# Kernel tuning notes

Hardware: AMD Instinct MI355X
Metric: run time of the kernel (lower is better)

The kernel has to match this reference:

```python
import jax, jax.numpy as jnp
import numpy as np

B, N, D, C = 4, 8192, 256, 1000
EPS = 1e-5


def expmap0(x, c=-1.0, eps=EPS):
    # Poincare-ball exponential map at the origin (matches torch version).
    x_norm = jnp.maximum(jnp.linalg.norm(x, axis=-1, keepdims=True), eps)
    curve_norm = jnp.sqrt(-c) * x_norm
    scale = jnp.tanh(curve_norm) / curve_norm
    return scale * x


def setup_inputs() -> dict:
    key = jax.random.key(0)
    k1, k2, k3 = jax.random.split(key, 3)
    features = jax.random.normal(k1, (B, N, D), dtype=jnp.float32)
    # kaiming-uniform-like scale for a 256-fan-in linear / embedding table
    lim = 1.0 / np.sqrt(D)
    W = jax.random.uniform(k2, (D, D), dtype=jnp.float32, minval=-lim, maxval=lim)
    b = jnp.zeros((D,), dtype=jnp.float32)
    embeddings = jax.random.uniform(k3, (C, D), dtype=jnp.float32, minval=-lim, maxval=lim)
    logit_scale = jnp.zeros((), dtype=jnp.float32)  # log(1.0)
    return {"features": features, "W": W, "b": b,
            "embeddings": embeddings, "logit_scale": logit_scale}


def reference(features, W, b, embeddings, logit_scale):
    # projection (nn.Linear): y = x @ W^T + b
    x = jnp.einsum("bnd,ed->bne", features, W) + b
    # map features and prototypes onto the Poincare ball (curvature = -1)
    x = expmap0(x)                       # [B, N, D], norms < 1
    protos = expmap0(embeddings)         # [C, D],    norms < 1

    # pairwise Poincare distance, computed via the norm expansion
    x_sq = jnp.sum(x * x, axis=-1)               # [B, N]
    p_sq = jnp.sum(protos * protos, axis=-1)     # [C]
    xp = jnp.einsum("bnd,cd->bnc", x, protos)    # [B, N, C]
    diff_sq = jnp.maximum(x_sq[..., None] + p_sq[None, None, :] - 2.0 * xp, 0.0)

    denom = jnp.maximum((1.0 - x_sq)[..., None] * (1.0 - p_sq)[None, None, :], EPS)
    argument = jnp.maximum(1.0 + 2.0 * diff_sq / denom, 1.0 + EPS)
    dists = jnp.arccosh(argument)                # [B, N, C]

    scale = jnp.minimum(jnp.exp(logit_scale), 100.0)
    return -dists * scale
```

## Files before the change

kernel.cpp:

```cpp
#include <hip/hip_runtime.h>
#include <hip/hip_fp16.h>


#define EPSF 1e-5f

typedef _Float16 half8 __attribute__((ext_vector_type(8)));
typedef _Float16 half4v __attribute__((ext_vector_type(4)));
typedef float f32x4 __attribute__((ext_vector_type(4)));

typedef __attribute__((address_space(3))) unsigned int as3_u32;
typedef __attribute__((address_space(1))) unsigned int as1_u32;
#define GLOAD16(gp, lp) __builtin_amdgcn_global_load_lds(  \
    (const as1_u32*)(gp), (as3_u32*)(lp), 16, 0, 0)

static __device__ __forceinline__ f32x4 mfma16(half8 a, half8 b, f32x4 c) {
  return __builtin_amdgcn_mfma_f32_16x16x32_f16(a, b, c, 0, 0, 0);
}

#define PROTO_OFF 0
#define PSQ_OFF   (1024 * 512)
#define WS_BYTES  (PSQ_OFF + 4096)

__global__ __launch_bounds__(256) void prep_kernel(const float* __restrict__ emb,
                                                   char* __restrict__ ws) {
  const int tid = threadIdx.x;
  const int wave = tid >> 6, lane = tid & 63;
  const int row = blockIdx.x * 4 + wave;
  float4 v = {0.f, 0.f, 0.f, 0.f};
  if (row < 1000) v = ((const float4*)emb)[row * 64 + lane];
  float s = v.x * v.x + v.y * v.y + v.z * v.z + v.w * v.w;
#pragma unroll
  for (int m = 1; m < 64; m <<= 1) s += __shfl_xor(s, m, 64);
  float r  = sqrtf(s);
  float rc = fmaxf(r, EPSF);
  float e  = __expf(2.0f * rc);
  float t  = 1.0f - 2.0f / (e + 1.0f);
  float sc = t / rc;
  float ps = t * t;
  if (row >= 1000) { sc = 0.0f; ps = 0.0f; }
  half4v h;
  h[0] = (_Float16)(v.x * sc); h[1] = (_Float16)(v.y * sc);
  h[2] = (_Float16)(v.z * sc); h[3] = (_Float16)(v.w * sc);
  const int byte = (lane * 8) ^ ((row & 7) << 4);
  *(half4v*)(ws + PROTO_OFF + row * 512 + byte) = h;
  if (lane == 0) ((float*)(ws + PSQ_OFF))[row] = ps;
}

__global__ __launch_bounds__(256, 2) void fused_kernel(
    const float* __restrict__ fea, const float* __restrict__ W,
    const float* __restrict__ bvec, const float* __restrict__ lsc,
    const char* __restrict__ ws, float* __restrict__ out) {
  __shared__ char lds[65536];
  char* buf0 = lds;
  char* buf1 = lds + 32768;

  const int tid  = threadIdx.x;
  const int w    = tid >> 6, lane = tid & 63;
  const int g = lane >> 4, i = lane & 15;
  const int xr = (i & 7) << 4;
  const int m0 = blockIdx.x * 64;

  const char*  pimg  = ws + PROTO_OFF;
  const float* psq_g = (const float*)(ws + PSQ_OFF);

  const f32x4 z4 = {0.f, 0.f, 0.f, 0.f};
  f32x4 accW[16];
#pragma unroll
  for (int cf = 0; cf < 16; ++cf) accW[cf] = z4;

  auto stageW = [&](int c, char* dst) {
#pragma unroll
    for (int p = 0; p < 8; ++p) {
      const int u = p * 256 + tid;
      const int n = u >> 3, k8 = u & 7;
      const float4* src = (const float4*)(W + (size_t)n * 256 + c * 64 + k8 * 8);
      float4 v0 = src[0], v1 = src[1];
      half8 h = {(_Float16)v0.x, (_Float16)v0.y, (_Float16)v0.z, (_Float16)v0.w,
                 (_Float16)v1.x, (_Float16)v1.y, (_Float16)v1.z, (_Float16)v1.w};
      *(half8*)(dst + n * 128 + ((k8 * 16) ^ ((n & 7) << 4))) = h;
    }
  };
  auto mfmaW = [&](int c, const char* bsrc) {
#pragma unroll
    for (int ksl = 0; ksl < 2; ++ksl) {
      const float4* ap = (const float4*)(fea +
          (size_t)(m0 + w * 16 + i) * 256 + c * 64 + ksl * 32 + g * 8);
      float4 a0 = ap[0], a1 = ap[1];
      half8 a = {(_Float16)a0.x, (_Float16)a0.y, (_Float16)a0.z, (_Float16)a0.w,
                 (_Float16)a1.x, (_Float16)a1.y, (_Float16)a1.z, (_Float16)a1.w};
#pragma unroll
      for (int cf = 0; cf < 16; ++cf) {
        half8 b = *(const half8*)(bsrc + (cf * 16 + i) * 128 +
                                  ((ksl * 64 + g * 16) ^ xr));
        accW[cf] = mfma16(a, b, accW[cf]);
      }
    }
  };

  stageW(0, buf0); __syncthreads();
  stageW(1, buf1); mfmaW(0, buf0); __syncthreads();
  stageW(2, buf0); mfmaW(1, buf1); __syncthreads();
  stageW(3, buf1); mfmaW(2, buf0); __syncthreads();
  mfmaW(3, buf1);  __syncthreads();

  auto stageP = [&](int nt, char* dst) {
#pragma unroll
    for (int p = 0; p < 8; ++p) {
      const int chunk = p * 4 + w;
      GLOAD16(pimg + (size_t)nt * 32768 + chunk * 1024 + lane * 16,
              dst + chunk * 1024);
    }
  };
  stageP(0, buf1);

  float ssum[4] = {0.f, 0.f, 0.f, 0.f};
#pragma unroll
  for (int cf = 0; cf < 16; ++cf) {
    const float bc = bvec[cf * 16 + i];
#pragma unroll
    for (int r = 0; r < 4; ++r) {
      accW[cf][r] += bc;
      ssum[r] = fmaf(accW[cf][r], accW[cf][r], ssum[r]);
    }
  }
#pragma unroll
  for (int m = 1; m < 16; m <<= 1)
#pragma unroll
    for (int r = 0; r < 4; ++r) ssum[r] += __shfl_xor(ssum[r], m, 64);

  float scl[4], xsv[4];
#pragma unroll
  for (int r = 0; r < 4; ++r) {
    float rn = sqrtf(ssum[r]);
    float rc = fmaxf(rn, EPSF);
    float e  = __expf(2.0f * rc);
    float t  = 1.0f - 2.0f / (e + 1.0f);
    scl[r] = t / rc;
    xsv[r] = t * t;
  }

  char* xsl = buf0 + w * 8192;
#pragma unroll
  for (int cf = 0; cf < 16; ++cf)
#pragma unroll
    for (int r = 0; r < 4; ++r) {
      const int row = g * 4 + r;
      *(_Float16*)(xsl + row * 512 + (((cf * 16 + i) * 2) ^ ((row & 7) << 4))) =
          (_Float16)(accW[cf][r] * scl[r]);
    }
  half8 A[8];
#pragma unroll
  for (int ks = 0; ks < 8; ++ks)
    A[ks] = *(const half8*)(xsl + i * 512 + ((ks * 64 + g * 16) ^ xr));

  const float sc_ln2 = fminf(__expf(lsc[0]), 100.0f) * 0.69314718055994531f;

  asm volatile("s_waitcnt vmcnt(0) lgkmcnt(0)" ::: "memory");
  __builtin_amdgcn_s_barrier();
  __builtin_amdgcn_sched_barrier(0);

  auto stepP = [&](int nt, const char* cur, char* nxt) {
    float psq[4];
#pragma unroll
    for (int cf = 0; cf < 4; ++cf) psq[cf] = psq_g[nt * 64 + cf * 16 + i];

    if (nt < 15) stageP(nt + 1, nxt);

    f32x4 acc[4] = {z4, z4, z4, z4};
#pragma unroll
    for (int ks = 0; ks < 8; ++ks) {
#pragma unroll
      for (int cf = 0; cf < 4; ++cf) {
        half8 b = *(const half8*)(cur + (cf * 16 + i) * 512 +
                                  ((ks * 64 + g * 16) ^ xr));
        acc[cf] = mfma16(A[ks], b, acc[cf]);
      }
    }
#pragma unroll
    for (int cf = 0; cf < 4; ++cf) {
      const float ps = psq[cf], omp = 1.0f - ps;
      const int col = nt * 64 + cf * 16 + i;
#pragma unroll
      for (int r = 0; r < 4; ++r) {
        const float xs   = xsv[r];
        const float diff = fmaxf(fmaf(-2.0f, acc[cf][r], xs + ps), 0.0f);
        const float den  = fmaxf((1.0f - xs) * omp, EPSF);
        const float arg  = fmaxf(fmaf(2.0f * diff, __builtin_amdgcn_rcpf(den), 1.0f),
                                 1.0f + EPSF);
        const float sq   = __builtin_amdgcn_sqrtf(fmaf(arg, arg, -1.0f));
        const float dist = __log2f(arg + sq);
        if (col < 1000)
          out[(size_t)(m0 + w * 16 + g * 4 + r) * 1000 + col] = -dist * sc_ln2;
      }
    }
    if (nt < 15) {
      asm volatile("s_waitcnt vmcnt(16)" ::: "memory");
      __builtin_amdgcn_s_barrier();
      __builtin_amdgcn_sched_barrier(0);
    }
  };

  for (int nt2 = 0; nt2 < 16; nt2 += 2) {
    stepP(nt2,     buf1, buf0);
    stepP(nt2 + 1, buf0, buf1);
  }
}

__global__ __launch_bounds__(256) void fallback_kernel(
    const float* __restrict__ fea, const float* __restrict__ W,
    const float* __restrict__ b, const float* __restrict__ emb,
    const float* __restrict__ lsc, float* __restrict__ out) {
  __shared__ float fr_[16][256];
  __shared__ float xr_[16][256];
  __shared__ float xs_[16];
  const int tid  = threadIdx.x;
  const int row0 = blockIdx.x * 16;

  for (int u = tid; u < 16 * 256; u += 256)
    fr_[u >> 8][u & 255] = fea[(size_t)(row0 + (u >> 8)) * 256 + (u & 255)];
  __syncthreads();

  float acc[16];
  const float bj = b[tid];
#pragma unroll
  for (int r = 0; r < 16; ++r) acc[r] = bj;
  for (int k = 0; k < 256; ++k) {
    const float wv = W[(size_t)tid * 256 + k];
#pragma unroll
    for (int r = 0; r < 16; ++r) acc[r] = fmaf(fr_[r][k], wv, acc[r]);
  }
#pragma unroll
  for (int r = 0; r < 16; ++r) xr_[r][tid] = acc[r];
  __syncthreads();

  if (tid < 16) {
    float s = 0.f;
    for (int k = 0; k < 256; ++k) s = fmaf(xr_[tid][k], xr_[tid][k], s);
    const float rn = sqrtf(s), rc = fmaxf(rn, EPSF);
    const float e = __expf(2.f * rc), t = 1.f - 2.f / (e + 1.f);
    xs_[tid] = t * t;
    fr_[tid][0] = t / rc;
  }
  __syncthreads();
  for (int u = tid; u < 16 * 256; u += 256)
    xr_[u >> 8][u & 255] *= fr_[u >> 8][0];
  __syncthreads();

  const float sc_out = fminf(__expf(lsc[0]), 100.0f);
  for (int c = tid; c < 1000; c += 256) {
    float s = 0.f;
    for (int k = 0; k < 256; ++k) {
      const float e0 = emb[(size_t)c * 256 + k];
      s = fmaf(e0, e0, s);
    }
    const float rn = sqrtf(s), rc = fmaxf(rn, EPSF);
    const float e = __expf(2.f * rc), t = 1.f - 2.f / (e + 1.f);
    const float psc = t / rc, ps = t * t, omp = 1.f - ps;
    float dots[16];
#pragma unroll
    for (int r = 0; r < 16; ++r) dots[r] = 0.f;
    for (int k = 0; k < 256; ++k) {
      const float pk = emb[(size_t)c * 256 + k] * psc;
#pragma unroll
      for (int r = 0; r < 16; ++r) dots[r] = fmaf(xr_[r][k], pk, dots[r]);
    }
#pragma unroll
    for (int r = 0; r < 16; ++r) {
      const float xs = xs_[r];
      const float diff = fmaxf(xs + ps - 2.f * dots[r], 0.f);
      const float den  = fmaxf((1.f - xs) * omp, EPSF);
      const float arg  = fmaxf(1.f + 2.f * diff / den, 1.f + EPSF);
      const float d    = logf(arg + sqrtf(fmaf(arg, arg, -1.f)));
      out[(size_t)(row0 + r) * 1000 + c] = -d * sc_out;
    }
  }
}

extern "C" void kernel_launch(void* const* d_in, const int* in_sizes, int n_in,
                              void* d_out, int out_size, void* d_ws, size_t ws_size,
                              hipStream_t stream) {
  (void)in_sizes; (void)n_in; (void)out_size;
  const float* fea = (const float*)d_in[0];
  const float* W   = (const float*)d_in[1];
  const float* b   = (const float*)d_in[2];
  const float* emb = (const float*)d_in[3];
  const float* ls  = (const float*)d_in[4];
  float* out = (float*)d_out;
  char*  ws  = (char*)d_ws;

  if (ws_size >= (size_t)WS_BYTES) {
    prep_kernel<<<256, 256, 0, stream>>>(emb, ws);
    fused_kernel<<<512, 256, 0, stream>>>(fea, W, b, ls, ws, out);
  } else {
    fallback_kernel<<<2048, 256, 0, stream>>>(fea, W, b, emb, ls, out);
  }
}
```

Measured before the change: 190.2 us.

## Split fused kernel across 8 waves with column halves and LDS-shared norms

Doubles the block to 512 threads, giving each pair of waves one 16-row strip, with each wave handling half of the projection output columns and half of the prototype columns. Partial squared norms are exchanged through LDS to finish the expmap scale. Prototype squared norms are staged in LDS once instead of being read from global memory every tile. The goal is more waves per CU to hide latency in the distance phase. The cost is more barriers and 70 KB of dynamic LDS per block, which caps blocks per CU and may contradict the 4-block launch bound.

```diff
diff --git a/kernel.cpp b/kernel.cpp
--- a/kernel.cpp
+++ b/kernel.cpp
@@ -8,11 +8,18 @@
 typedef _Float16 half4v __attribute__((ext_vector_type(4)));
 typedef float f32x4 __attribute__((ext_vector_type(4)));
 
+typedef __attribute__((address_space(3))) char as3_char;
 typedef __attribute__((address_space(3))) unsigned int as3_u32;
 typedef __attribute__((address_space(1))) unsigned int as1_u32;
 #define GLOAD16(gp, lp) __builtin_amdgcn_global_load_lds(  \
     (const as1_u32*)(gp), (as3_u32*)(lp), 16, 0, 0)
 
+#define LDS_H8(off)  (*((__attribute__((address_space(3)))       half8*)((as3_char*)lds + (off))))
+#define LDS_CH8(off) (*((__attribute__((address_space(3))) const half8*)((as3_char*)lds + (off))))
+#define LDS_F16(off) (*((__attribute__((address_space(3)))    _Float16*)((as3_char*)lds + (off))))
+#define LDS_F32(off) (*((__attribute__((address_space(3)))       float*)((as3_char*)lds + (off))))
+#define LDS_V4(off)  (*((__attribute__((address_space(3)))       f32x4*)((as3_char*)lds + (off))))
+
 static __device__ __forceinline__ f32x4 mfma16(half8 a, half8 b, f32x4 c) {
   return __builtin_amdgcn_mfma_f32_16x16x32_f16(a, b, c, 0, 0, 0);
 }
@@ -20,6 +27,10 @@
 #define PROTO_OFF 0
 #define PSQ_OFF   (1024 * 512)
 #define WS_BYTES  (PSQ_OFF + 4096)
+
+#define PSQ_L   65536
+#define PSUM_L  69632
+#define LDS_SZ  70144
 
 __global__ __launch_bounds__(256) void prep_kernel(const float* __restrict__ emb,
                                                    char* __restrict__ ws) {
@@ -46,163 +57,176 @@
   if (lane == 0) ((float*)(ws + PSQ_OFF))[row] = ps;
 }
 
-__global__ __launch_bounds__(256, 2) void fused_kernel(
+__global__ __launch_bounds__(512, 4) void fused_kernel(
     const float* __restrict__ fea, const float* __restrict__ W,
     const float* __restrict__ bvec, const float* __restrict__ lsc,
     const char* __restrict__ ws, float* __restrict__ out) {
-  __shared__ char lds[65536];
-  char* buf0 = lds;
-  char* buf1 = lds + 32768;
-
+  extern __shared__ char lds[];
   const int tid  = threadIdx.x;
-  const int w    = tid >> 6, lane = tid & 63;
+  const int wave = tid >> 6, lane = tid & 63;
+  const int r = wave >> 1, c = wave & 1;
   const int g = lane >> 4, i = lane & 15;
   const int xr = (i & 7) << 4;
+  const int ht = r * 64 + lane;
   const int m0 = blockIdx.x * 64;
-
-  const char*  pimg  = ws + PROTO_OFF;
-  const float* psq_g = (const float*)(ws + PSQ_OFF);
+  const int cbase = c * 32768;
+
+  const char* pimg = ws + PROTO_OFF;
+
+  float bl[8];
+#pragma unroll
+  for (int cf = 0; cf < 8; ++cf) bl[cf] = bvec[c * 128 + cf * 16 + i];
+  const float sc_ln2 = fminf(__expf(lsc[0]), 100.0f) * 0.69314718055994531f;
+  if (tid < 256) {
+    f32x4 pq = ((const f32x4*)(ws + PSQ_OFF))[tid];
+    LDS_V4(PSQ_L + tid * 16) = pq;
+  }
 
   const f32x4 z4 = {0.f, 0.f, 0.f, 0.f};
-  f32x4 accW[16];
-#pragma unroll
-  for (int cf = 0; cf < 16; ++cf) accW[cf] = z4;
-
-  auto stageW = [&](int c, char* dst) {
-#pragma unroll
-    for (int p = 0; p < 8; ++p) {
-      const int u = p * 256 + tid;
-      const int n = u >> 3, k8 = u & 7;
-      const float4* src = (const float4*)(W + (size_t)n * 256 + c * 64 + k8 * 8);
+  f32x4 accW[8];
+#pragma unroll
+  for (int cf = 0; cf < 8; ++cf) accW[cf] = z4;
+
+  auto stageW = [&](int kc, int boff) {
+#pragma unroll
+    for (int p = 0; p < 4; ++p) {
+      const int u = p * 256 + ht;
+      const int nl = u >> 3, k8 = u & 7;
+      const float4* src = (const float4*)(W + (size_t)(c * 128 + nl) * 256 +
+                                          kc * 64 + k8 * 8);
       float4 v0 = src[0], v1 = src[1];
       half8 h = {(_Float16)v0.x, (_Float16)v0.y, (_Float16)v0.z, (_Float16)v0.w,
                  (_Float16)v1.x, (_Float16)v1.y, (_Float16)v1.z, (_Float16)v1.w};
-      *(half8*)(dst + n * 128 + ((k8 * 16) ^ ((n & 7) << 4))) = h;
+      LDS_H8(boff + nl * 128 + ((k8 * 16) ^ ((nl & 7) << 4))) = h;
     }
   };
-  auto mfmaW = [&](int c, const char* bsrc) {
+  auto mfmaW = [&](int kc, int boff) {
 #pragma unroll
     for (int ksl = 0; ksl < 2; ++ksl) {
-      const float4* ap = (const float4*)(fea +
-          (size_t)(m0 + w * 16 + i) * 256 + c * 64 + ksl * 32 + g * 8);
+      const float4* ap = (const float4*)(fea + (size_t)(m0 + r * 16 + i) * 256 +
+                                         kc * 64 + ksl * 32 + g * 8);
       float4 a0 = ap[0], a1 = ap[1];
       half8 a = {(_Float16)a0.x, (_Float16)a0.y, (_Float16)a0.z, (_Float16)a0.w,
                  (_Float16)a1.x, (_Float16)a1.y, (_Float16)a1.z, (_Float16)a1.w};
 #pragma unroll
-      for (int cf = 0; cf < 16; ++cf) {
-        half8 b = *(const half8*)(bsrc + (cf * 16 + i) * 128 +
-                                  ((ksl * 64 + g * 16) ^ xr));
+      for (int cf = 0; cf < 8; ++cf) {
+        half8 b = LDS_CH8(boff + (cf * 16 + i) * 128 + ((ksl * 64 + g * 16) ^ xr));
         accW[cf] = mfma16(a, b, accW[cf]);
       }
     }
   };
 
-  stageW(0, buf0); __syncthreads();
-  stageW(1, buf1); mfmaW(0, buf0); __syncthreads();
-  stageW(2, buf0); mfmaW(1, buf1); __syncthreads();
-  stageW(3, buf1); mfmaW(2, buf0); __syncthreads();
-  mfmaW(3, buf1);  __syncthreads();
-
-  auto stageP = [&](int nt, char* dst) {
-#pragma unroll
-    for (int p = 0; p < 8; ++p) {
-      const int chunk = p * 4 + w;
-      GLOAD16(pimg + (size_t)nt * 32768 + chunk * 1024 + lane * 16,
-              dst + chunk * 1024);
-    }
-  };
-  stageP(0, buf1);
+  stageW(0, cbase);         __syncthreads();
+  stageW(1, cbase + 16384); mfmaW(0, cbase);         __syncthreads();
+  stageW(2, cbase);         mfmaW(1, cbase + 16384); __syncthreads();
+  stageW(3, cbase + 16384); mfmaW(2, cbase);         __syncthreads();
+  mfmaW(3, cbase + 16384);  __syncthreads();
 
   float ssum[4] = {0.f, 0.f, 0.f, 0.f};
 #pragma unroll
-  for (int cf = 0; cf < 16; ++cf) {
-    const float bc = bvec[cf * 16 + i];
-#pragma unroll
-    for (int r = 0; r < 4; ++r) {
-      accW[cf][r] += bc;
-      ssum[r] = fmaf(accW[cf][r], accW[cf][r], ssum[r]);
-    }
-  }
+  for (int cf = 0; cf < 8; ++cf)
+#pragma unroll
+    for (int reg = 0; reg < 4; ++reg) {
+      accW[cf][reg] += bl[cf];
+      ssum[reg] = fmaf(accW[cf][reg], accW[cf][reg], ssum[reg]);
+    }
 #pragma unroll
   for (int m = 1; m < 16; m <<= 1)
 #pragma unroll
-    for (int r = 0; r < 4; ++r) ssum[r] += __shfl_xor(ssum[r], m, 64);
+    for (int reg = 0; reg < 4; ++reg) ssum[reg] += __shfl_xor(ssum[reg], m, 64);
+  if (i == 0) {
+#pragma unroll
+    for (int reg = 0; reg < 4; ++reg)
+      LDS_F32(PSUM_L + (c * 64 + r * 16 + g * 4 + reg) * 4) = ssum[reg];
+  }
+  __syncthreads();
 
   float scl[4], xsv[4];
 #pragma unroll
-  for (int r = 0; r < 4; ++r) {
-    float rn = sqrtf(ssum[r]);
+  for (int reg = 0; reg < 4; ++reg) {
+    const int row = r * 16 + g * 4 + reg;
+    float s  = LDS_F32(PSUM_L + row * 4) + LDS_F32(PSUM_L + (64 + row) * 4);
+    float rn = sqrtf(s);
     float rc = fmaxf(rn, EPSF);
     float e  = __expf(2.0f * rc);
     float t  = 1.0f - 2.0f / (e + 1.0f);
-    scl[r] = t / rc;
-    xsv[r] = t * t;
-  }
-
-  char* xsl = buf0 + w * 8192;
-#pragma unroll
-  for (int cf = 0; cf < 16; ++cf)
-#pragma unroll
-    for (int r = 0; r < 4; ++r) {
-      const int row = g * 4 + r;
-      *(_Float16*)(xsl + row * 512 + (((cf * 16 + i) * 2) ^ ((row & 7) << 4))) =
-          (_Float16)(accW[cf][r] * scl[r]);
-    }
+    scl[reg] = t / rc;
+    xsv[reg] = t * t;
+  }
+
+#pragma unroll
+  for (int cf = 0; cf < 8; ++cf)
+#pragma unroll
+    for (int reg = 0; reg < 4; ++reg) {
+      const int row = r * 16 + g * 4 + reg;
+      const int col = c * 128 + cf * 16 + i;
+      LDS_F16(row * 512 + ((col * 2) ^ ((row & 7) << 4))) =
+          (_Float16)(accW[cf][reg] * scl[reg]);
+    }
+  __syncthreads();
   half8 A[8];
 #pragma unroll
   for (int ks = 0; ks < 8; ++ks)
-    A[ks] = *(const half8*)(xsl + i * 512 + ((ks * 64 + g * 16) ^ xr));
-
-  const float sc_ln2 = fminf(__expf(lsc[0]), 100.0f) * 0.69314718055994531f;
-
-  asm volatile("s_waitcnt vmcnt(0) lgkmcnt(0)" ::: "memory");
+    A[ks] = LDS_CH8((r * 16 + i) * 512 + ((ks * 64 + g * 16) ^ xr));
+  asm volatile("s_waitcnt lgkmcnt(0)" ::: "memory");
+  __builtin_amdgcn_sched_barrier(0);
+  __syncthreads();
+
+  auto stageP = [&](int t, int boff) {
+#pragma unroll
+    for (int p = 0; p < 4; ++p) {
+      const int chunk = p * 4 + r;
+      GLOAD16(pimg + ((size_t)(c * 512 + t * 32) * 512) + chunk * 1024 + lane * 16,
+              (as3_char*)lds + boff + chunk * 1024);
+    }
+  };
+  stageP(0, cbase);
+  asm volatile("s_waitcnt vmcnt(0)" ::: "memory");
   __builtin_amdgcn_s_barrier();
   __builtin_amdgcn_sched_barrier(0);
 
-  auto stepP = [&](int nt, const char* cur, char* nxt) {
-    float psq[4];
-#pragma unroll
-    for (int cf = 0; cf < 4; ++cf) psq[cf] = psq_g[nt * 64 + cf * 16 + i];
-
-    if (nt < 15) stageP(nt + 1, nxt);
-
-    f32x4 acc[4] = {z4, z4, z4, z4};
-#pragma unroll
-    for (int ks = 0; ks < 8; ++ks) {
-#pragma unroll
-      for (int cf = 0; cf < 4; ++cf) {
-        half8 b = *(const half8*)(cur + (cf * 16 + i) * 512 +
-                                  ((ks * 64 + g * 16) ^ xr));
+  for (int t = 0; t < 16; ++t) {
+    const int cur = cbase + (t & 1) * 16384;
+    const int nxt = cbase + ((t + 1) & 1) * 16384;
+
+    float psq[2];
+#pragma unroll
+    for (int cf = 0; cf < 2; ++cf)
+      psq[cf] = LDS_F32(PSQ_L + (c * 512 + t * 32 + cf * 16 + i) * 4);
+
+    if (t < 15) stageP(t + 1, nxt);
+
+    f32x4 acc[2] = {z4, z4};
+#pragma unroll
+    for (int ks = 0; ks < 8; ++ks)
+#pragma unroll
+      for (int cf = 0; cf < 2; ++cf) {
+        half8 b = LDS_CH8(cur + (cf * 16 + i) * 512 + ((ks * 64 + g * 16) ^ xr));
         acc[cf] = mfma16(A[ks], b, acc[cf]);
       }
-    }
-#pragma unroll
-    for (int cf = 0; cf < 4; ++cf) {
+
+#pragma unroll
+    for (int cf = 0; cf < 2; ++cf) {
       const float ps = psq[cf], omp = 1.0f - ps;
-      const int col = nt * 64 + cf * 16 + i;
-#pragma unroll
-      for (int r = 0; r < 4; ++r) {
-        const float xs   = xsv[r];
-        const float diff = fmaxf(fmaf(-2.0f, acc[cf][r], xs + ps), 0.0f);
+      const int col = c * 512 + t * 32 + cf * 16 + i;
+#pragma unroll
+      for (int reg = 0; reg < 4; ++reg) {
+        const float xs   = xsv[reg];
+        const float diff = fmaxf(fmaf(-2.0f, acc[cf][reg], xs + ps), 0.0f);
         const float den  = fmaxf((1.0f - xs) * omp, EPSF);
         const float arg  = fmaxf(fmaf(2.0f * diff, __builtin_amdgcn_rcpf(den), 1.0f),
                                  1.0f + EPSF);
         const float sq   = __builtin_amdgcn_sqrtf(fmaf(arg, arg, -1.0f));
         const float dist = __log2f(arg + sq);
         if (col < 1000)
-          out[(size_t)(m0 + w * 16 + g * 4 + r) * 1000 + col] = -dist * sc_ln2;
+          out[(size_t)(m0 + r * 16 + g * 4 + reg) * 1000 + col] = -dist * sc_ln2;
       }
     }
-    if (nt < 15) {
-      asm volatile("s_waitcnt vmcnt(16)" ::: "memory");
+    if (t < 15) {
+      asm volatile("s_waitcnt vmcnt(8)" ::: "memory");
       __builtin_amdgcn_s_barrier();
       __builtin_amdgcn_sched_barrier(0);
     }
-  };
-
-  for (int nt2 = 0; nt2 < 16; nt2 += 2) {
-    stepP(nt2,     buf1, buf0);
-    stepP(nt2 + 1, buf0, buf1);
   }
 }
 
@@ -247,10 +271,10 @@
   __syncthreads();
 
   const float sc_out = fminf(__expf(lsc[0]), 100.0f);
-  for (int c = tid; c < 1000; c += 256) {
+  for (int cc = tid; cc < 1000; cc += 256) {
     float s = 0.f;
     for (int k = 0; k < 256; ++k) {
-      const float e0 = emb[(size_t)c * 256 + k];
+      const float e0 = emb[(size_t)cc * 256 + k];
       s = fmaf(e0, e0, s);
     }
     const float rn = sqrtf(s), rc = fmaxf(rn, EPSF);
@@ -260,7 +284,7 @@
 #pragma unroll
     for (int r = 0; r < 16; ++r) dots[r] = 0.f;
     for (int k = 0; k < 256; ++k) {
-      const float pk = emb[(size_t)c * 256 + k] * psc;
+      const float pk = emb[(size_t)cc * 256 + k] * psc;
 #pragma unroll
       for (int r = 0; r < 16; ++r) dots[r] = fmaf(xr_[r][k], pk, dots[r]);
     }
@@ -271,7 +295,7 @@
       const float den  = fmaxf((1.f - xs) * omp, EPSF);
       const float arg  = fmaxf(1.f + 2.f * diff / den, 1.f + EPSF);
       const float d    = logf(arg + sqrtf(fmaf(arg, arg, -1.f)));
-      out[(size_t)(row0 + r) * 1000 + c] = -d * sc_out;
+      out[(size_t)(row0 + r) * 1000 + cc] = -d * sc_out;
     }
   }
 }
@@ -289,8 +313,10 @@
   char*  ws  = (char*)d_ws;
 
   if (ws_size >= (size_t)WS_BYTES) {
+    (void)hipFuncSetAttribute((const void*)fused_kernel,
+                              hipFuncAttributeMaxDynamicSharedMemorySize, LDS_SZ);
     prep_kernel<<<256, 256, 0, stream>>>(emb, ws);
-    fused_kernel<<<512, 256, 0, stream>>>(fea, W, b, ls, ws, out);
+    fused_kernel<<<512, 512, LDS_SZ, stream>>>(fea, W, b, ls, ws, out);
   } else {
     fallback_kernel<<<2048, 256, 0, stream>>>(fea, W, b, emb, ls, out);
   }
```

After: 195.2 us. 1.03x slower.
